# Kernel optimization log

Hardware: AMD Instinct MI355X
Metric: run time of the kernel (lower is better)

## Reference

```python
import jax, jax.numpy as jnp
import numpy as np

B, L_DEC, L_ENC = 4, 1024, 1024
D_MODEL, D_INNER, N_HEAD, D_K, D_V = 512, 256, 8, 64, 64
TEMP = D_K ** 0.5
EPS = 1e-6


def _layernorm(x, g, b):
    mu = jnp.mean(x, axis=-1, keepdims=True)
    var = jnp.mean(jnp.square(x - mu), axis=-1, keepdims=True)
    return (x - mu) * jax.lax.rsqrt(var + EPS) * g + b


def _mha(x_q, x_kv, Wq, Wk, Wv, Wfc, ln_g, ln_b, mask):
    # Faithful to source: only the query input is layer-normed; k/v use raw x_kv.
    resid = x_q
    qn = _layernorm(x_q, ln_g, ln_b)
    # Stacked per-head projections: Wq/Wk/Wv are [H, d_k, d_model]
    q = jnp.einsum('bld,hkd->bhlk', qn, Wq) / TEMP   # [B,H,Lq,dk]
    k = jnp.einsum('bld,hkd->bhlk', x_kv, Wk)        # [B,H,Lk,dk]
    v = jnp.einsum('bld,hkd->bhlk', x_kv, Wv)        # [B,H,Lk,dv]
    scores = jnp.einsum('bhqd,bhkd->bhqk', q, k)     # [B,H,Lq,Lk]
    if mask is not None:
        scores = jnp.where(mask[:, None, :, :] == 0, -jnp.inf, scores)
    attn = jax.nn.softmax(scores, axis=-1)
    out = jnp.einsum('bhqk,bhkd->bhqd', attn, v)     # [B,H,Lq,dv]
    Bq, H, Lq, dv = out.shape
    out = out.transpose(0, 2, 1, 3).reshape(Bq, Lq, H * dv)
    return out @ Wfc.T + resid


def _ffn(x, W1, b1, W2, b2, ln_g, ln_b):
    resid = x
    h = _layernorm(x, ln_g, ln_b)
    h = jax.nn.relu(h @ W1.T + b1) @ W2.T + b2
    return h + resid


def setup_inputs() -> dict:
    key = jax.random.key(0)
    ks = jax.random.split(key, 20)
    s = 0.02
    dec_input = jax.random.normal(ks[0], (B, L_DEC, D_MODEL), jnp.float32)
    enc_output = jax.random.normal(ks[1], (B, L_ENC, D_MODEL), jnp.float32)
    slf_attn_mask = jnp.tril(jnp.ones((1, L_DEC, L_DEC), jnp.int32))  # causal
    p = {}
    for i, pre in enumerate(['slf', 'enc']):
        base = 2 + i * 4
        p[f'{pre}_Wq'] = jax.random.normal(ks[base], (N_HEAD, D_K, D_MODEL), jnp.float32) * s
        p[f'{pre}_Wk'] = jax.random.normal(ks[base + 1], (N_HEAD, D_K, D_MODEL), jnp.float32) * s
        p[f'{pre}_Wv'] = jax.random.normal(ks[base + 2], (N_HEAD, D_V, D_MODEL), jnp.float32) * s
        p[f'{pre}_Wfc'] = jax.random.normal(ks[base + 3], (D_MODEL, N_HEAD * D_V), jnp.float32) * s
        p[f'{pre}_ln_g'] = jnp.ones((D_MODEL,), jnp.float32)
        p[f'{pre}_ln_b'] = jnp.zeros((D_MODEL,), jnp.float32)
    p['ffn_W1'] = jax.random.normal(ks[10], (D_INNER, D_MODEL), jnp.float32) * s
    p['ffn_b1'] = jnp.zeros((D_INNER,), jnp.float32)
    p['ffn_W2'] = jax.random.normal(ks[11], (D_MODEL, D_INNER), jnp.float32) * s
    p['ffn_b2'] = jnp.zeros((D_MODEL,), jnp.float32)
    p['ffn_ln_g'] = jnp.ones((D_MODEL,), jnp.float32)
    p['ffn_ln_b'] = jnp.zeros((D_MODEL,), jnp.float32)
    return {'dec_input': dec_input, 'enc_output': enc_output,
            'slf_attn_mask': slf_attn_mask, **p}


def reference(dec_input, enc_output,
              slf_Wq, slf_Wk, slf_Wv, slf_Wfc, slf_ln_g, slf_ln_b,
              enc_Wq, enc_Wk, enc_Wv, enc_Wfc, enc_ln_g, enc_ln_b,
              ffn_W1, ffn_b1, ffn_W2, ffn_b2, ffn_ln_g, ffn_ln_b,
              slf_attn_mask):
    x = _mha(dec_input, dec_input, slf_Wq, slf_Wk, slf_Wv, slf_Wfc,
             slf_ln_g, slf_ln_b, slf_attn_mask)
    x = _mha(x, enc_output, enc_Wq, enc_Wk, enc_Wv, enc_Wfc,
             enc_ln_g, enc_ln_b, None)
    x = _ffn(x, ffn_W1, ffn_b1, ffn_W2, ffn_b2, ffn_ln_g, ffn_ln_b)
    return x
```

## Files before the change

### kernel.cpp

```cpp
#include <hip/hip_runtime.h>
#include <hip/hip_bf16.h>
#include <math.h>

#define DMODEL 512
#define NHEAD  8
#define DHEAD  64

typedef __attribute__((ext_vector_type(8))) short bf16x8;
typedef __attribute__((ext_vector_type(4))) float f32x4;
typedef __attribute__((ext_vector_type(4))) short short4v;

static __device__ inline short f2bf(float f) {
    __hip_bfloat16 h = __float2bfloat16(f);
    return *reinterpret_cast<short*>(&h);
}

#define GLOAD_LDS16(gp, lp)                                                      \
    __builtin_amdgcn_global_load_lds(                                            \
        (const __attribute__((address_space(1))) unsigned int*)(gp),             \
        (__attribute__((address_space(3))) unsigned int*)(lp), 16, 0, 0)

struct CvtArgs {
    const float* src[12];
    short*       dst[12];
    int          n[12];
    int          start[12];
};

__global__ __launch_bounds__(256) void cvt_kernel(CvtArgs args) {
    int bid = blockIdx.x;
    int t = 0;
    while (t < 11 && bid >= args.start[t + 1]) ++t;
    int idx = ((bid - args.start[t]) * 256 + threadIdx.x) * 8;
    if (idx >= args.n[t]) return;
    const float* s = args.src[t] + idx;
    float4 a = *(const float4*)s;
    float4 b = *(const float4*)(s + 4);
    bf16x8 o;
    o[0] = f2bf(a.x); o[1] = f2bf(a.y); o[2] = f2bf(a.z); o[3] = f2bf(a.w);
    o[4] = f2bf(b.x); o[5] = f2bf(b.y); o[6] = f2bf(b.z); o[7] = f2bf(b.w);
    *(bf16x8*)(args.dst[t] + idx) = o;
}

__global__ __launch_bounds__(256) void ln_kernel(const float* __restrict__ X,
                                                 const float* __restrict__ gam,
                                                 const float* __restrict__ bet,
                                                 short* __restrict__ Y) {
    int row = blockIdx.x * 4 + (threadIdx.x >> 6);
    int tid = threadIdx.x & 63;
    const float* x = X + (size_t)row * DMODEL;
    float4 a = *(const float4*)(x + tid * 4);
    float4 b = *(const float4*)(x + 256 + tid * 4);
    float sum = a.x + a.y + a.z + a.w + b.x + b.y + b.z + b.w;
    float sq  = a.x*a.x + a.y*a.y + a.z*a.z + a.w*a.w
              + b.x*b.x + b.y*b.y + b.z*b.z + b.w*b.w;
#pragma unroll
    for (int off = 1; off < 64; off <<= 1) {
        sum += __shfl_xor(sum, off);
        sq  += __shfl_xor(sq, off);
    }
    float mu  = sum * (1.0f / DMODEL);
    float var = sq * (1.0f / DMODEL) - mu * mu;
    float r   = rsqrtf(var + 1e-6f);

    float4 g1 = *(const float4*)(gam + tid * 4);
    float4 c1 = *(const float4*)(bet + tid * 4);
    float4 g2 = *(const float4*)(gam + 256 + tid * 4);
    float4 c2 = *(const float4*)(bet + 256 + tid * 4);
    short4v y1, y2;
    y1.x = f2bf((a.x - mu) * r * g1.x + c1.x);
    y1.y = f2bf((a.y - mu) * r * g1.y + c1.y);
    y1.z = f2bf((a.z - mu) * r * g1.z + c1.z);
    y1.w = f2bf((a.w - mu) * r * g1.w + c1.w);
    y2.x = f2bf((b.x - mu) * r * g2.x + c2.x);
    y2.y = f2bf((b.y - mu) * r * g2.y + c2.y);
    y2.z = f2bf((b.z - mu) * r * g2.z + c2.z);
    y2.w = f2bf((b.w - mu) * r * g2.w + c2.w);
    short* y = Y + (size_t)row * DMODEL;
    *(short4v*)(y + tid * 4)       = y1;
    *(short4v*)(y + 256 + tid * 4) = y2;
}

struct GJobs {
    const short* A[3];
    const short* W[3];
    const float* bias[3];
    const float* resid[3];
    void*        C[3];
    int M[3], N[3], K[3];
    float scale[3];
    int relu[3], obf[3], nblk[3];
};

__global__ __launch_bounds__(256) void gemm_bf16(GJobs jb) {
    __shared__ short As[2][64 * 64];
    __shared__ short Bs[2][64 * 64];

    int bid = blockIdx.x, j = 0;
    while (j < 2 && bid >= jb.nblk[j]) { bid -= jb.nblk[j]; ++j; }
    const short* __restrict__ A = jb.A[j];
    const short* __restrict__ W = jb.W[j];
    const int N = jb.N[j], K = jb.K[j];
    {
        int nb = jb.nblk[j];
        if ((nb & 7) == 0) bid = (bid & 7) * (nb >> 3) + (bid >> 3);
    }
    const int nbx = N >> 6;
    const int tn = (bid % nbx) * 64;
    const int tm = (bid / nbx) * 64;

    const int tid  = threadIdx.x;
    const int w    = tid >> 6;
    const int l    = tid & 63;
    const int lq   = l & 15;
    const int g    = l >> 4;
    const int wm   = (w >> 1) * 32;
    const int wn   = (w & 1) * 32;
    const int lrow = l >> 3;
    const int lsl  = l & 7;

    f32x4 acc[2][2];
#pragma unroll
    for (int i = 0; i < 2; ++i)
#pragma unroll
        for (int jj = 0; jj < 2; ++jj)
            acc[i][jj] = (f32x4){0.f, 0.f, 0.f, 0.f};

    const int nkt = K >> 6;

#pragma unroll
    for (int i = 0; i < 2; ++i) {
        int row = i * 32 + w * 8 + lrow;
        int slot = lsl ^ (row & 7);
        GLOAD_LDS16(A + (size_t)(tm + row) * K + slot * 8,
                    &As[0][i * 2048 + w * 512]);
        GLOAD_LDS16(W + (size_t)(tn + row) * K + slot * 8,
                    &Bs[0][i * 2048 + w * 512]);
    }

#pragma unroll 2
    for (int kt = 0; kt < nkt; ++kt) {
        const int cur = kt & 1;
        __syncthreads();
        if (kt + 1 < nkt) {
            const int k0n = (kt + 1) * 64;
#pragma unroll
            for (int i = 0; i < 2; ++i) {
                int row = i * 32 + w * 8 + lrow;
                int slot = lsl ^ (row & 7);
                GLOAD_LDS16(A + (size_t)(tm + row) * K + k0n + slot * 8,
                            &As[cur ^ 1][i * 2048 + w * 512]);
                GLOAD_LDS16(W + (size_t)(tn + row) * K + k0n + slot * 8,
                            &Bs[cur ^ 1][i * 2048 + w * 512]);
            }
        }

#pragma unroll
        for (int ks = 0; ks < 2; ++ks) {
            const int sl = ((ks * 4 + g) ^ (lq & 7)) * 8;
            bf16x8 af[2], bfv[2];
#pragma unroll
            for (int i = 0; i < 2; ++i) {
                af[i]  = *(const bf16x8*)&As[cur][(wm + i * 16 + lq) * 64 + sl];
                bfv[i] = *(const bf16x8*)&Bs[cur][(wn + i * 16 + lq) * 64 + sl];
            }
#pragma unroll
            for (int i = 0; i < 2; ++i)
#pragma unroll
                for (int jj = 0; jj < 2; ++jj)
                    acc[i][jj] = __builtin_amdgcn_mfma_f32_16x16x32_bf16(
                        af[i], bfv[jj], acc[i][jj], 0, 0, 0);
        }
    }

    const float* bias  = jb.bias[j];
    const float* resid = jb.resid[j];
    const float scale  = jb.scale[j];
    const int relu = jb.relu[j], obf = jb.obf[j];
#pragma unroll
    for (int i = 0; i < 2; ++i) {
#pragma unroll
        for (int r = 0; r < 4; ++r) {
            int row = tm + wm + i * 16 + g * 4 + r;
#pragma unroll
            for (int jj = 0; jj < 2; ++jj) {
                int col = tn + wn + jj * 16 + lq;
                float v = acc[i][jj][r] * scale;
                if (bias)  v += bias[col];
                if (resid) v += resid[(size_t)row * N + col];
                if (relu)  v = fmaxf(v, 0.f);
                if (obf) ((short*)jb.C[j])[(size_t)row * N + col] = f2bf(v);
                else     ((float*)jb.C[j])[(size_t)row * N + col] = v;
            }
        }
    }
}

__global__ __launch_bounds__(512) void attn_mfma_kernel(
        const short* __restrict__ Q, const short* __restrict__ K,
        const short* __restrict__ V, short* __restrict__ O,
        int Lq, int Lk, int causal, int qs, int kvs) {
    __shared__ short Kt[2][64 * 64];
    __shared__ short Vt[2][64][72];
    __shared__ short Pb[8][16][72];

    const int tid  = threadIdx.x;
    const int wave = tid >> 6;
    const int wq4  = wave & 3;
    const int tsel = wave >> 2;
    const int lane = tid & 63;
    const int lq   = lane & 15;
    const int g    = lane >> 4;
    const int bh   = blockIdx.y;
    const int b = bh >> 3, h = bh & 7;
    const int qx = causal ? ((int)gridDim.x - 1 - (int)blockIdx.x) : (int)blockIdx.x;
    const int q0 = qx * 64 + wq4 * 16;
    const float NEG = -__builtin_inff();

    size_t qoff = (size_t)(b * Lq + q0 + lq) * qs + h * DHEAD;
    bf16x8 qf0 = *(const bf16x8*)(Q + qoff + g * 8);
    bf16x8 qf1 = *(const bf16x8*)(Q + qoff + 32 + g * 8);

    f32x4 o[4] = {{0,0,0,0},{0,0,0,0},{0,0,0,0},{0,0,0,0}};
    f32x4 lacc = {0.f, 0.f, 0.f, 0.f};

    bf16x8 ones;
    {
        short ov = (lq == 0) ? (short)0x3F80 : (short)0;
#pragma unroll
        for (int i = 0; i < 8; ++i) ones[i] = ov;
    }

    const int nkt = causal ? (qx + 1) : (Lk >> 6);
    const int npair = (nkt + 1) >> 1;
    const int lrow = lane >> 3;
    const int lsl  = lane & 7;
    const int gt = tid & 255;
    const int va = gt & 31;
    const int vd = (gt >> 5) * 8;

#pragma unroll 1
    for (int kp = 0; kp < npair; ++kp) {
        const int t = 2 * kp + tsel;
        const int active = (t < nkt);
        __syncthreads();
        if (active) {
#pragma unroll
            for (int i = 0; i < 2; ++i) {
                int row = i * 32 + wq4 * 8 + lrow;
                int slot = lsl ^ (row & 7);
                GLOAD_LDS16(K + (size_t)(b * Lk + t * 64 + row) * kvs + h * DHEAD + slot * 8,
                            &Kt[tsel][i * 2048 + wq4 * 512]);
            }
            size_t gb = (size_t)(b * Lk + t * 64 + 2 * va) * kvs + h * DHEAD + vd;
            bf16x8 v0 = *(const bf16x8*)(V + gb);
            bf16x8 v1 = *(const bf16x8*)(V + gb + kvs);
#pragma unroll
            for (int i = 0; i < 8; ++i) {
                unsigned p = (unsigned short)v0[i] | ((unsigned)(unsigned short)v1[i] << 16);
                *(unsigned*)&Vt[tsel][vd + i][2 * va] = p;
            }
        }
        __syncthreads();
        if (!active) continue;

        f32x4 s[4];
#pragma unroll
        for (int sub = 0; sub < 4; ++sub) {
            int rr = sub * 16 + lq;
            const int sl0 = ((0 + g) ^ (lq & 7)) * 8;
            const int sl1 = ((4 + g) ^ (lq & 7)) * 8;
            bf16x8 kf0 = *(const bf16x8*)&Kt[tsel][rr * 64 + sl0];
            bf16x8 kf1 = *(const bf16x8*)&Kt[tsel][rr * 64 + sl1];
            f32x4 a = {0.f, 0.f, 0.f, 0.f};
            a = __builtin_amdgcn_mfma_f32_16x16x32_bf16(kf0, qf0, a, 0, 0, 0);
            a = __builtin_amdgcn_mfma_f32_16x16x32_bf16(kf1, qf1, a, 0, 0, 0);
            s[sub] = a;
        }
        if (causal && t == nkt - 1) {
            int qg = q0 + lq;
#pragma unroll
            for (int sub = 0; sub < 4; ++sub) {
#pragma unroll
                for (int r = 0; r < 4; ++r) {
                    int kg = t * 64 + sub * 16 + g * 4 + r;
                    if (kg > qg) s[sub][r] = NEG;
                }
            }
        }

#pragma unroll
        for (int sub = 0; sub < 4; ++sub) {
            short4v p4;
            p4.x = f2bf(__expf(fminf(s[sub][0], 60.f)));
            p4.y = f2bf(__expf(fminf(s[sub][1], 60.f)));
            p4.z = f2bf(__expf(fminf(s[sub][2], 60.f)));
            p4.w = f2bf(__expf(fminf(s[sub][3], 60.f)));
            *(short4v*)&Pb[wave][lq][sub * 16 + g * 4] = p4;
        }
        bf16x8 pf0 = *(const bf16x8*)&Pb[wave][lq][g * 8];
        bf16x8 pf1 = *(const bf16x8*)&Pb[wave][lq][32 + g * 8];

#pragma unroll
        for (int dc = 0; dc < 4; ++dc) {
            bf16x8 vf0 = *(const bf16x8*)&Vt[tsel][dc * 16 + lq][g * 8];
            bf16x8 vf1 = *(const bf16x8*)&Vt[tsel][dc * 16 + lq][32 + g * 8];
            o[dc] = __builtin_amdgcn_mfma_f32_16x16x32_bf16(pf0, vf0, o[dc], 0, 0, 0);
            o[dc] = __builtin_amdgcn_mfma_f32_16x16x32_bf16(pf1, vf1, o[dc], 0, 0, 0);
        }
        lacc = __builtin_amdgcn_mfma_f32_16x16x32_bf16(pf0, ones, lacc, 0, 0, 0);
        lacc = __builtin_amdgcn_mfma_f32_16x16x32_bf16(pf1, ones, lacc, 0, 0, 0);
    }

    float* Ox = (float*)&Pb[0][0][0];
    float* Lx = Ox + 4 * 16 * 64;
    __syncthreads();
    if (tsel == 1) {
#pragma unroll
        for (int r = 0; r < 4; ++r) {
            int row = g * 4 + r;
            float* dst = Ox + (wq4 * 16 + row) * 64;
            dst[lq]      = o[0][r];
            dst[16 + lq] = o[1][r];
            dst[32 + lq] = o[2][r];
            dst[48 + lq] = o[3][r];
            if (lq == 0) Lx[wq4 * 16 + row] = lacc[r];
        }
    }
    __syncthreads();
    if (tsel == 0) {
#pragma unroll
        for (int r = 0; r < 4; ++r) {
            int row = g * 4 + r;
            float lr = __shfl(lacc[r], g << 4) + Lx[wq4 * 16 + row];
            float inv = 1.f / lr;
            const float* srcx = Ox + (wq4 * 16 + row) * 64;
            size_t ob = (size_t)(b * Lq + q0 + row) * qs + h * DHEAD + lq;
            O[ob + 0]  = f2bf((o[0][r] + srcx[lq])      * inv);
            O[ob + 16] = f2bf((o[1][r] + srcx[16 + lq]) * inv);
            O[ob + 32] = f2bf((o[2][r] + srcx[32 + lq]) * inv);
            O[ob + 48] = f2bf((o[3][r] + srcx[48 + lq]) * inv);
        }
    }
}

static void launch_gemm(GJobs& jb, int njobs, hipStream_t stream) {
    int total = 0;
    for (int i = 0; i < 3; ++i) { if (i >= njobs) jb.nblk[i] = 0; total += jb.nblk[i]; }
    gemm_bf16<<<total, 256, 0, stream>>>(jb);
}

extern "C" void kernel_launch(void* const* d_in, const int* in_sizes, int n_in,
                              void* d_out, int out_size, void* d_ws, size_t ws_size,
                              hipStream_t stream) {
    const float* dec       = (const float*)d_in[0];
    const float* enc       = (const float*)d_in[1];
    const float* slf_Wq    = (const float*)d_in[3];
    const float* slf_Wk    = (const float*)d_in[4];
    const float* slf_Wv    = (const float*)d_in[5];
    const float* slf_Wfc   = (const float*)d_in[6];
    const float* slf_ln_g  = (const float*)d_in[7];
    const float* slf_ln_b  = (const float*)d_in[8];
    const float* enc_Wq    = (const float*)d_in[9];
    const float* enc_Wk    = (const float*)d_in[10];
    const float* enc_Wv    = (const float*)d_in[11];
    const float* enc_Wfc   = (const float*)d_in[12];
    const float* enc_ln_g  = (const float*)d_in[13];
    const float* enc_ln_b  = (const float*)d_in[14];
    const float* ffn_W1    = (const float*)d_in[15];
    const float* ffn_b1    = (const float*)d_in[16];
    const float* ffn_W2    = (const float*)d_in[17];
    const float* ffn_b2    = (const float*)d_in[18];
    const float* ffn_ln_g  = (const float*)d_in[19];
    const float* ffn_ln_b  = (const float*)d_in[20];
    float* out = (float*)d_out;

    const int Bb = 4, L = 1024, M = Bb * L;
    const size_t NE = (size_t)M * DMODEL;
    const int WQN = NHEAD * DHEAD * DMODEL;
    float* ws = (float*)d_ws;
    float* x1 = ws;
    float* x2 = ws + NE;
    short* kv16e = (short*)x2;
    short* sb = (short*)(ws + 2 * NE);
    short* dec16 = sb;               sb += NE;
    short* enc16 = sb;               sb += NE;
    short* qn16  = sb;               sb += NE;
    short* q16   = sb;               sb += NE;
    short* ao16  = sb;               sb += NE;
    short* kv16  = sb;               sb += 2 * NE;
    short* h16   = sb;               sb += NE / 2;
    short* wq_s  = sb;               sb += WQN;
    short* wkv_s = sb;               sb += 2 * WQN;
    short* wfc_s = sb;               sb += WQN;
    short* wq_e  = sb;               sb += WQN;
    short* wkv_e = sb;               sb += 2 * WQN;
    short* wfc_e = sb;               sb += WQN;
    short* w1_16 = sb;               sb += 256 * DMODEL;
    short* w2_16 = sb;               sb += DMODEL * 256;

    CvtArgs ca;
    ca.src[0] = dec;     ca.dst[0] = dec16;         ca.n[0] = (int)NE;
    ca.src[1] = enc;     ca.dst[1] = enc16;         ca.n[1] = (int)NE;
    ca.src[2] = slf_Wq;  ca.dst[2] = wq_s;          ca.n[2] = WQN;
    ca.src[3] = slf_Wk;  ca.dst[3] = wkv_s;         ca.n[3] = WQN;
    ca.src[4] = slf_Wv;  ca.dst[4] = wkv_s + WQN;   ca.n[4] = WQN;
    ca.src[5] = slf_Wfc; ca.dst[5] = wfc_s;         ca.n[5] = WQN;
    ca.src[6] = enc_Wq;  ca.dst[6] = wq_e;          ca.n[6] = WQN;
    ca.src[7] = enc_Wk;  ca.dst[7] = wkv_e;         ca.n[7] = WQN;
    ca.src[8] = enc_Wv;  ca.dst[8] = wkv_e + WQN;   ca.n[8] = WQN;
    ca.src[9] = enc_Wfc; ca.dst[9] = wfc_e;         ca.n[9] = WQN;
    ca.src[10] = ffn_W1; ca.dst[10] = w1_16;        ca.n[10] = 256 * DMODEL;
    ca.src[11] = ffn_W2; ca.dst[11] = w2_16;        ca.n[11] = DMODEL * 256;
    {
        int acc = 0;
        for (int t = 0; t < 12; ++t) { ca.start[t] = acc; acc += ca.n[t] / 2048; }
        cvt_kernel<<<acc, 256, 0, stream>>>(ca);
    }

    dim3 attn_grid(L / 64, Bb * NHEAD);
    const int NB512  = (M / 64) * (512 / 64);
    const int NB1024 = (M / 64) * (1024 / 64);
    const int NB256  = (M / 64) * (256 / 64);

    ln_kernel<<<M / 4, 256, 0, stream>>>(dec, slf_ln_g, slf_ln_b, qn16);
    {
        GJobs jb = {};
        jb.A[0] = qn16;  jb.W[0] = wq_s;  jb.C[0] = q16;
        jb.M[0] = M; jb.N[0] = 512;  jb.K[0] = 512; jb.scale[0] = 0.125f;
        jb.obf[0] = 1; jb.nblk[0] = NB512;
        jb.A[1] = dec16; jb.W[1] = wkv_s; jb.C[1] = kv16;
        jb.M[1] = M; jb.N[1] = 1024; jb.K[1] = 512; jb.scale[1] = 1.f;
        jb.obf[1] = 1; jb.nblk[1] = NB1024;
        jb.A[2] = enc16; jb.W[2] = wkv_e; jb.C[2] = kv16e;
        jb.M[2] = M; jb.N[2] = 1024; jb.K[2] = 512; jb.scale[2] = 1.f;
        jb.obf[2] = 1; jb.nblk[2] = NB1024;
        launch_gemm(jb, 3, stream);
    }
    attn_mfma_kernel<<<attn_grid, 512, 0, stream>>>(q16, kv16, kv16 + 512, ao16,
                                                    L, L, 1, DMODEL, 1024);
    {
        GJobs jb = {};
        jb.A[0] = ao16; jb.W[0] = wfc_s; jb.resid[0] = dec; jb.C[0] = x1;
        jb.M[0] = M; jb.N[0] = 512; jb.K[0] = 512; jb.scale[0] = 1.f;
        jb.obf[0] = 0; jb.nblk[0] = NB512;
        launch_gemm(jb, 1, stream);
    }

    ln_kernel<<<M / 4, 256, 0, stream>>>(x1, enc_ln_g, enc_ln_b, qn16);
    {
        GJobs jb = {};
        jb.A[0] = qn16; jb.W[0] = wq_e; jb.C[0] = q16;
        jb.M[0] = M; jb.N[0] = 512; jb.K[0] = 512; jb.scale[0] = 0.125f;
        jb.obf[0] = 1; jb.nblk[0] = NB512;
        launch_gemm(jb, 1, stream);
    }
    attn_mfma_kernel<<<attn_grid, 512, 0, stream>>>(q16, kv16e, kv16e + 512, ao16,
                                                    L, L, 0, DMODEL, 1024);
    {
        GJobs jb = {};
        jb.A[0] = ao16; jb.W[0] = wfc_e; jb.resid[0] = x1; jb.C[0] = x2;
        jb.M[0] = M; jb.N[0] = 512; jb.K[0] = 512; jb.scale[0] = 1.f;
        jb.obf[0] = 0; jb.nblk[0] = NB512;
        launch_gemm(jb, 1, stream);
    }

    ln_kernel<<<M / 4, 256, 0, stream>>>(x2, ffn_ln_g, ffn_ln_b, qn16);
    {
        GJobs jb = {};
        jb.A[0] = qn16; jb.W[0] = w1_16; jb.bias[0] = ffn_b1; jb.C[0] = h16;
        jb.M[0] = M; jb.N[0] = 256; jb.K[0] = 512; jb.scale[0] = 1.f;
        jb.relu[0] = 1; jb.obf[0] = 1; jb.nblk[0] = NB256;
        launch_gemm(jb, 1, stream);
    }
    {
        GJobs jb = {};
        jb.A[0] = h16; jb.W[0] = w2_16; jb.bias[0] = ffn_b2; jb.resid[0] = x2;
        jb.C[0] = out;
        jb.M[0] = M; jb.N[0] = 512; jb.K[0] = 256; jb.scale[0] = 1.f;
        jb.obf[0] = 0; jb.nblk[0] = NB512;
        launch_gemm(jb, 1, stream);
    }
}
```

Baseline: 238.6 us.

## Double-buffer K tiles and prefetch next V tile into registers in attention

Adds a second K buffer in LDS per tile-select group so the async global-to-LDS load of the next K tile is issued before computing on the current one. The next V tile is prefetched into registers and only transposed into LDS at the start of the following iteration. This aims to overlap global memory latency with MFMA compute, at the cost of doubling K shared memory (which may reduce occupancy) and extra live registers.

```diff
diff --git a/kernel.cpp b/kernel.cpp
--- a/kernel.cpp
+++ b/kernel.cpp
@@ -200,7 +200,7 @@
         const short* __restrict__ Q, const short* __restrict__ K,
         const short* __restrict__ V, short* __restrict__ O,
         int Lq, int Lk, int causal, int qs, int kvs) {
-    __shared__ short Kt[2][64 * 64];
+    __shared__ short Kt[2][2][64 * 64];
     __shared__ short Vt[2][64][72];
     __shared__ short Pb[8][16][72];
 
@@ -238,40 +238,61 @@
     const int gt = tid & 255;
     const int va = gt & 31;
     const int vd = (gt >> 5) * 8;
+    const size_t kvh = (size_t)(b * Lk) * kvs + h * DHEAD;
+
+    bf16x8 vna, vnb;
+    if (tsel < nkt) {
+#pragma unroll
+        for (int i = 0; i < 2; ++i) {
+            int row = i * 32 + wq4 * 8 + lrow;
+            int slot = lsl ^ (row & 7);
+            GLOAD_LDS16(K + kvh + (size_t)(tsel * 64 + row) * kvs + slot * 8,
+                        &Kt[tsel][0][i * 2048 + wq4 * 512]);
+        }
+        size_t gb = kvh + (size_t)(tsel * 64 + 2 * va) * kvs + vd;
+        vna = *(const bf16x8*)(V + gb);
+        vnb = *(const bf16x8*)(V + gb + kvs);
+    }
 
 #pragma unroll 1
     for (int kp = 0; kp < npair; ++kp) {
+        const int cur = kp & 1;
         const int t = 2 * kp + tsel;
         const int active = (t < nkt);
         __syncthreads();
         if (active) {
 #pragma unroll
+            for (int i = 0; i < 8; ++i) {
+                unsigned p = (unsigned short)vna[i] | ((unsigned)(unsigned short)vnb[i] << 16);
+                *(unsigned*)&Vt[tsel][vd + i][2 * va] = p;
+            }
+        }
+        __syncthreads();
+
+        const int tn = t + 2;
+        if (tn < nkt) {
+#pragma unroll
             for (int i = 0; i < 2; ++i) {
                 int row = i * 32 + wq4 * 8 + lrow;
                 int slot = lsl ^ (row & 7);
-                GLOAD_LDS16(K + (size_t)(b * Lk + t * 64 + row) * kvs + h * DHEAD + slot * 8,
-                            &Kt[tsel][i * 2048 + wq4 * 512]);
+                GLOAD_LDS16(K + kvh + (size_t)(tn * 64 + row) * kvs + slot * 8,
+                            &Kt[tsel][cur ^ 1][i * 2048 + wq4 * 512]);
             }
-            size_t gb = (size_t)(b * Lk + t * 64 + 2 * va) * kvs + h * DHEAD + vd;
-            bf16x8 v0 = *(const bf16x8*)(V + gb);
-            bf16x8 v1 = *(const bf16x8*)(V + gb + kvs);
-#pragma unroll
-            for (int i = 0; i < 8; ++i) {
-                unsigned p = (unsigned short)v0[i] | ((unsigned)(unsigned short)v1[i] << 16);
-                *(unsigned*)&Vt[tsel][vd + i][2 * va] = p;
-            }
-        }
-        __syncthreads();
+            size_t gb = kvh + (size_t)(tn * 64 + 2 * va) * kvs + vd;
+            vna = *(const bf16x8*)(V + gb);
+            vnb = *(const bf16x8*)(V + gb + kvs);
+        }
         if (!active) continue;
 
+        const short* KT = &Kt[tsel][cur][0];
         f32x4 s[4];
 #pragma unroll
         for (int sub = 0; sub < 4; ++sub) {
             int rr = sub * 16 + lq;
             const int sl0 = ((0 + g) ^ (lq & 7)) * 8;
             const int sl1 = ((4 + g) ^ (lq & 7)) * 8;
-            bf16x8 kf0 = *(const bf16x8*)&Kt[tsel][rr * 64 + sl0];
-            bf16x8 kf1 = *(const bf16x8*)&Kt[tsel][rr * 64 + sl1];
+            bf16x8 kf0 = *(const bf16x8*)&KT[rr * 64 + sl0];
+            bf16x8 kf1 = *(const bf16x8*)&KT[rr * 64 + sl1];
             f32x4 a = {0.f, 0.f, 0.f, 0.f};
             a = __builtin_amdgcn_mfma_f32_16x16x32_bf16(kf0, qf0, a, 0, 0, 0);
             a = __builtin_amdgcn_mfma_f32_16x16x32_bf16(kf1, qf1, a, 0, 0, 0);
```

Result: slower. 247.0 us (+3.5%).
